# Performance work log

Measured on AMD Instinct MI355X. Metric: run time of the kernel, lower is better.

## Reference

```python
import jax, jax.numpy as jnp
import numpy as np

N_NODES = 100000
N_EDGES = 1600000
N_FEAT = 128
HIDN = 256
N_CLASSES = 47


def setup_inputs() -> dict:
    key = jax.random.key(0)
    ks = jax.random.split(key, 8)
    x = jax.random.normal(ks[0], (N_NODES, N_FEAT), dtype=jnp.float32)
    edge_index = jax.random.randint(ks[1], (2, N_EDGES), 0, N_NODES, dtype=jnp.int32)
    s1 = 1.0 / np.sqrt(N_FEAT)
    s2 = 1.0 / np.sqrt(HIDN)
    Wl1 = jax.random.normal(ks[2], (N_FEAT, HIDN), dtype=jnp.float32) * s1
    Wr1 = jax.random.normal(ks[3], (N_FEAT, HIDN), dtype=jnp.float32) * s1
    b1 = jnp.zeros((HIDN,), dtype=jnp.float32)
    Wl2 = jax.random.normal(ks[4], (HIDN, N_CLASSES), dtype=jnp.float32) * s2
    Wr2 = jax.random.normal(ks[5], (HIDN, N_CLASSES), dtype=jnp.float32) * s2
    b2 = jnp.zeros((N_CLASSES,), dtype=jnp.float32)
    return {"x": x, "edge_index": edge_index, "Wl1": Wl1, "Wr1": Wr1, "b1": b1,
            "Wl2": Wl2, "Wr2": Wr2, "b2": b2}


def _sage_conv(x, src, dst, Wl, Wr, b):
    # PyG SAGEConv (mean aggr): out = lin_l(mean_{j->i} x_j) + lin_r(x_i)
    n = x.shape[0]
    msg = x[src]                                                   # [E, F] gather
    agg = jax.ops.segment_sum(msg, dst, num_segments=n)            # [N, F]
    deg = jax.ops.segment_sum(jnp.ones((src.shape[0], 1), x.dtype), dst,
                              num_segments=n)                      # [N, 1]
    mean = agg / jnp.maximum(deg, 1.0)
    return mean @ Wl + b + x @ Wr


def reference(x, edge_index, Wl1, Wr1, b1, Wl2, Wr2, b2):
    src, dst = edge_index[0], edge_index[1]
    h = _sage_conv(x, src, dst, Wl1, Wr1, b1)
    h = jax.nn.relu(h)
    # dropout omitted (eval mode / deterministic baseline)
    out = _sage_conv(h, src, dst, Wl2, Wr2, b2)
    return out
```

## Files before the change

kernel.cpp:

```cpp
#include <hip/hip_runtime.h>

#define NN 100000
#define NE 1600000
#define NF 128
#define NH 256
#define NC 47
#define NB 391
#define CH 8192
#define NCH ((NE + CH - 1) / CH)

#define PB_HIST 0
#define PB_CAST (PB_HIST + NCH)
#define NCAST   (NN * NF / 4 / 256)
#define PB_BT1  (PB_CAST + NCAST)
#define PB_BT2  (PB_BT1 + 256)
#define PB_END  (PB_BT2 + 96)

typedef __attribute__((ext_vector_type(8))) short bf16x8;
typedef __attribute__((ext_vector_type(4))) float f32x4;
typedef __attribute__((ext_vector_type(2))) float f32x2;

typedef __attribute__((address_space(1))) const void as1_void;
typedef __attribute__((address_space(3))) void as3_void;
__device__ __forceinline__ void gload16(const void* g, void* l) {
    __builtin_amdgcn_global_load_lds((as1_void*)g, (as3_void*)l, 16, 0, 0);
}

__device__ inline unsigned short f2bf(float f) {
    unsigned u = __builtin_bit_cast(unsigned, f);
    unsigned r = u + 0x7fffu + ((u >> 16) & 1u);
    return (unsigned short)(r >> 16);
}
__device__ inline float bfl(unsigned u) {
    return __builtin_bit_cast(float, u << 16);
}


__global__ __launch_bounds__(256) void prep_k(const int* __restrict__ dst,
                                              int* __restrict__ chunk_hist,
                                              int* __restrict__ total,
                                              const float* __restrict__ x,
                                              unsigned short* __restrict__ xb,
                                              unsigned* __restrict__ xq,
                                              const float* __restrict__ Wl1,
                                              const float* __restrict__ Wr1,
                                              unsigned short* __restrict__ Bt1,
                                              const float* __restrict__ Wl2,
                                              const float* __restrict__ Wr2,
                                              unsigned short* __restrict__ Bt2) {
    __shared__ int h[NB];
    int tid = threadIdx.x;
    int blk = blockIdx.x;
    if (blk < PB_CAST) {
        int ch = blk;
        for (int i = tid; i < NB; i += 256) h[i] = 0;
        __syncthreads();
        int e0 = ch * CH;
        int e1 = min(e0 + CH, NE);
        for (int e = e0 + tid; e < e1; e += 256)
            atomicAdd(&h[dst[e] >> 8], 1);
        __syncthreads();
        for (int i = tid; i < NB; i += 256) {
            int v = h[i];
            chunk_hist[(size_t)ch * NB + i] = v;
            if (v) atomicAdd(&total[i], v);
        }
    } else if (blk < PB_BT1) {
        int i = (blk - PB_CAST) * 256 + tid;
        float4 v = *reinterpret_cast<const float4*>(x + (size_t)i * 4);
        ushort4 o;
        o.x = f2bf(v.x); o.y = f2bf(v.y); o.z = f2bf(v.z); o.w = f2bf(v.w);
        *reinterpret_cast<ushort4*>(xb + (size_t)i * 4) = o;
        int r = __builtin_amdgcn_cvt_pk_fp8_f32(v.x, v.y, 0, false);
        r = __builtin_amdgcn_cvt_pk_fp8_f32(v.z, v.w, r, true);
        xq[i] = (unsigned)r;
    } else if (blk < PB_BT2) {
        int idx = (blk - PB_BT1) * 256 + tid;
        int n = idx >> 8, k = idx & 255;
        float v = (k < 128) ? Wl1[(size_t)k * NH + n] : Wr1[(size_t)(k - 128) * NH + n];
        Bt1[idx] = f2bf(v);
    } else {
        int idx = (blk - PB_BT2) * 256 + tid;
        int n = idx >> 8, k = idx & 255;
        float v = 0.f;
        if (n < 47) v = Wl2[(size_t)k * NC + n];
        else if (n >= 48 && n < 95) v = Wr2[(size_t)k * NC + (n - 48)];
        Bt2[idx] = f2bf(v);
    }
}


__global__ __launch_bounds__(64) void scancol_k(const int* __restrict__ chunk_hist,
                                                const int* __restrict__ total,
                                                int* __restrict__ bucket_base,
                                                int* __restrict__ chunk_off) {
    int b = blockIdx.x;
    int lane = threadIdx.x;
    int base = 0;
    for (int i0 = 0; i0 < NB; i0 += 64) {
        int i = i0 + lane;
        base += (i < b) ? total[i] : 0;
    }
    #pragma unroll
    for (int off = 1; off < 64; off <<= 1)
        base += __shfl_xor(base, off);
    if (lane == 0) bucket_base[b] = base;
    int run = base;
    for (int c0 = 0; c0 < NCH; c0 += 64) {
        int c = c0 + lane;
        int v = (c < NCH) ? chunk_hist[(size_t)c * NB + b] : 0;
        int s = v;
        #pragma unroll
        for (int off = 1; off < 64; off <<= 1) {
            int t = __shfl_up(s, off);
            if (lane >= off) s += t;
        }
        if (c < NCH) chunk_off[(size_t)c * NB + b] = run + s - v;
        run += __shfl(s, 63);
    }
}

__global__ __launch_bounds__(256) void scatter2_k(const int* __restrict__ src,
                                                  const int* __restrict__ dst,
                                                  const int* __restrict__ chunk_off,
                                                  unsigned* __restrict__ ebuf) {
    __shared__ int cur[NB];
    int tid = threadIdx.x, ch = blockIdx.x;
    for (int i = tid; i < NB; i += 256)
        cur[i] = chunk_off[(size_t)ch * NB + i];
    __syncthreads();
    int e0 = ch * CH;
    int e1 = min(e0 + CH, NE);
    for (int e = e0 + tid; e < e1; e += 256) {
        int d = dst[e];
        int b = d >> 8;
        int p = atomicAdd(&cur[b], 1);
        ebuf[p] = ((unsigned)(d & 255) << 24) | (unsigned)src[e];
    }
}

__global__ __launch_bounds__(256) void build_csr_k(const unsigned* __restrict__ ebuf,
                                                   const int* __restrict__ bucket_base,
                                                   const int* __restrict__ bucket_cnt,
                                                   int* __restrict__ row_start,
                                                   int* __restrict__ deg,
                                                   float* __restrict__ inv_deg,
                                                   int* __restrict__ csr_src) {
    __shared__ int s[256];
    __shared__ int cursor[256];
    int tid = threadIdx.x;
    int b = blockIdx.x;
    int lo = b << 8;
    int ebase = bucket_base[b];
    int ne = bucket_cnt[b];

    s[tid] = 0;
    __syncthreads();
    for (int e = tid; e < ne; e += 256)
        atomicAdd(&s[ebuf[ebase + e] >> 24], 1);
    __syncthreads();
    int v = s[tid];
    __syncthreads();
    for (int off = 1; off < 256; off <<= 1) {
        int t = (tid >= off) ? s[tid - off] : 0;
        __syncthreads();
        s[tid] += t;
        __syncthreads();
    }
    int excl = s[tid] - v;
    int node = lo + tid;
    if (node < NN) {
        row_start[node] = ebase + excl;
        deg[node] = v;
        inv_deg[node] = 1.0f / (float)(v > 1 ? v : 1);
    }
    cursor[tid] = ebase + excl;
    __syncthreads();
    for (int e = tid; e < ne; e += 256) {
        unsigned u = ebuf[ebase + e];
        int p = atomicAdd(&cursor[u >> 24], 1);
        csr_src[p] = (int)(u & 0xFFFFFFu);
    }
}


__global__ __launch_bounds__(256) void agg_mean_128q_k(const unsigned* __restrict__ xq,
                                                       const int* __restrict__ csr_src,
                                                       const int* __restrict__ row_start,
                                                       const int* __restrict__ deg,
                                                       const float* __restrict__ inv_deg,
                                                       unsigned short* __restrict__ mean1) {
    int node = blockIdx.x * 16 + (threadIdx.x >> 4);
    int l16 = threadIdx.x & 15;
    if (node >= NN) return;
    int s0 = row_start[node];
    int d  = deg[node];
    f32x2 acc[4];
    #pragma unroll
    for (int k = 0; k < 4; ++k) acc[k] = f32x2{0.f, 0.f};
    int j = 0;
    for (; j + 7 < d; j += 8) {
        uint2 w[8];
        #pragma unroll
        for (int r = 0; r < 8; ++r) {
            int s = csr_src[s0 + j + r];
            w[r] = *reinterpret_cast<const uint2*>(xq + (size_t)s * 32 + l16 * 2);
        }
        #pragma unroll
        for (int r = 0; r < 8; ++r) {
            acc[0] += __builtin_amdgcn_cvt_pk_f32_fp8((int)w[r].x, false);
            acc[1] += __builtin_amdgcn_cvt_pk_f32_fp8((int)w[r].x, true);
            acc[2] += __builtin_amdgcn_cvt_pk_f32_fp8((int)w[r].y, false);
            acc[3] += __builtin_amdgcn_cvt_pk_f32_fp8((int)w[r].y, true);
        }
    }
    for (; j + 3 < d; j += 4) {
        uint2 w[4];
        #pragma unroll
        for (int r = 0; r < 4; ++r) {
            int s = csr_src[s0 + j + r];
            w[r] = *reinterpret_cast<const uint2*>(xq + (size_t)s * 32 + l16 * 2);
        }
        #pragma unroll
        for (int r = 0; r < 4; ++r) {
            acc[0] += __builtin_amdgcn_cvt_pk_f32_fp8((int)w[r].x, false);
            acc[1] += __builtin_amdgcn_cvt_pk_f32_fp8((int)w[r].x, true);
            acc[2] += __builtin_amdgcn_cvt_pk_f32_fp8((int)w[r].y, false);
            acc[3] += __builtin_amdgcn_cvt_pk_f32_fp8((int)w[r].y, true);
        }
    }
    for (; j < d; ++j) {
        int s = csr_src[s0 + j];
        uint2 w = *reinterpret_cast<const uint2*>(xq + (size_t)s * 32 + l16 * 2);
        acc[0] += __builtin_amdgcn_cvt_pk_f32_fp8((int)w.x, false);
        acc[1] += __builtin_amdgcn_cvt_pk_f32_fp8((int)w.x, true);
        acc[2] += __builtin_amdgcn_cvt_pk_f32_fp8((int)w.y, false);
        acc[3] += __builtin_amdgcn_cvt_pk_f32_fp8((int)w.y, true);
    }
    float inv = inv_deg[node];
    bf16x8 o;
    #pragma unroll
    for (int k = 0; k < 4; ++k) {
        o[k * 2]     = (short)f2bf(acc[k].x * inv);
        o[k * 2 + 1] = (short)f2bf(acc[k].y * inv);
    }
    *reinterpret_cast<bf16x8*>(mean1 + (size_t)node * NF + l16 * 8) = o;
}

__global__ __launch_bounds__(256) void agg_mean_47q_add_k(const unsigned* __restrict__ tq,
                                                          const int* __restrict__ csr_src,
                                                          const int* __restrict__ row_start,
                                                          const int* __restrict__ deg,
                                                          const float* __restrict__ inv_deg,
                                                          float* __restrict__ out) {
    int node = blockIdx.x * 16 + (threadIdx.x >> 4);
    int l16 = threadIdx.x & 15;
    if (node >= NN) return;
    int s0 = row_start[node];
    int d  = deg[node];
    f32x2 a01 = {0.f, 0.f}, a23 = {0.f, 0.f};
    int j = 0;
    for (; j + 7 < d; j += 8) {
        unsigned w[8];
        #pragma unroll
        for (int r = 0; r < 8; ++r) {
            int s = csr_src[s0 + j + r];
            w[r] = tq[(size_t)s * 16 + l16];
        }
        #pragma unroll
        for (int r = 0; r < 8; ++r) {
            a01 += __builtin_amdgcn_cvt_pk_f32_fp8((int)w[r], false);
            a23 += __builtin_amdgcn_cvt_pk_f32_fp8((int)w[r], true);
        }
    }
    for (; j + 3 < d; j += 4) {
        unsigned w[4];
        #pragma unroll
        for (int r = 0; r < 4; ++r) {
            int s = csr_src[s0 + j + r];
            w[r] = tq[(size_t)s * 16 + l16];
        }
        #pragma unroll
        for (int r = 0; r < 4; ++r) {
            a01 += __builtin_amdgcn_cvt_pk_f32_fp8((int)w[r], false);
            a23 += __builtin_amdgcn_cvt_pk_f32_fp8((int)w[r], true);
        }
    }
    for (; j < d; ++j) {
        int s = csr_src[s0 + j];
        unsigned w = tq[(size_t)s * 16 + l16];
        a01 += __builtin_amdgcn_cvt_pk_f32_fp8((int)w, false);
        a23 += __builtin_amdgcn_cvt_pk_f32_fp8((int)w, true);
    }
    float inv = inv_deg[node];
    int c0 = l16 * 4;
    float vals[4] = {a01.x, a01.y, a23.x, a23.y};
    #pragma unroll
    for (int m = 0; m < 4; ++m) {
        int col = c0 + m;
        if (col < NC) {
            size_t o = (size_t)node * NC + col;
            out[o] += vals[m] * inv;
        }
    }
}


__global__ __launch_bounds__(256, 4) void gemm12_k(const unsigned short* __restrict__ mean1,
                                                   const unsigned short* __restrict__ xb,
                                                   const unsigned short* __restrict__ Bt1,
                                                   const float* __restrict__ b1,
                                                   const unsigned short* __restrict__ Bt2,
                                                   const float* __restrict__ b2,
                                                   unsigned char* __restrict__ tq,
                                                   float* __restrict__ out) {
    __shared__ __align__(16) union SM {
        struct { short As[2][64 * 32]; short Bs[2][256 * 32]; } g;
        unsigned short Hs[64 * 256];
    } sm;
    const int tid = threadIdx.x;
    const int row0 = blockIdx.x * 64;
    const int lane = tid & 63;
    const int wid = tid >> 6;
    const int r15 = lane & 15;
    const int kg = lane >> 4;
    const int swz = (kg ^ ((lane >> 1) & 3)) & 3;

    const int wc = wid;
    f32x4 acc[4][4];
    #pragma unroll
    for (int i = 0; i < 4; ++i)
        #pragma unroll
        for (int j = 0; j < 4; ++j)
            acc[i][j] = f32x4{0.f, 0.f, 0.f, 0.f};

    auto stage = [&](int buf, int kt) {
        {
            int row = tid >> 2, g = tid & 3;
            int grow = row0 + row;
            if (grow >= NN) grow = NN - 1;
            int gs = g ^ ((row >> 1) & 3);
            const unsigned short* asrc = (kt < 128) ? mean1 : xb;
            gload16(asrc + (size_t)grow * NF + (kt & 127) + gs * 8, &sm.g.As[buf][tid * 8]);
        }
        #pragma unroll
        for (int i = 0; i < 4; ++i) {
            int c = tid + i * 256;
            int rn = c >> 2, g = c & 3;
            int gs = g ^ ((rn >> 1) & 3);
            gload16(Bt1 + (size_t)rn * 256 + kt + gs * 8, &sm.g.Bs[buf][c * 8]);
        }
    };
    auto compute = [&](int buf) {
        bf16x8 a[4], b[4];
        #pragma unroll
        for (int mi = 0; mi < 4; ++mi)
            a[mi] = *reinterpret_cast<const bf16x8*>(&sm.g.As[buf][(mi * 16 + r15) * 32 + swz * 8]);
        #pragma unroll
        for (int ni = 0; ni < 4; ++ni)
            b[ni] = *reinterpret_cast<const bf16x8*>(&sm.g.Bs[buf][(wc * 64 + ni * 16 + r15) * 32 + swz * 8]);
        #pragma unroll
        for (int mi = 0; mi < 4; ++mi)
            #pragma unroll
            for (int ni = 0; ni < 4; ++ni)
                acc[mi][ni] = __builtin_amdgcn_mfma_f32_16x16x32_bf16(a[mi], b[ni], acc[mi][ni], 0, 0, 0);
    };

    stage(0, 0);
    __syncthreads();
    int cur = 0;
    #pragma unroll 1
    for (int ks = 0; ks < 8; ++ks) {
        if (ks + 1 < 8) stage(cur ^ 1, (ks + 1) * 32);
        compute(cur);
        __syncthreads();
        cur ^= 1;
    }

    #pragma unroll
    for (int ni = 0; ni < 4; ++ni) {
        int col = wc * 64 + ni * 16 + r15;
        float bias = b1[col];
        int kgrp = col >> 3, within = col & 7;
        #pragma unroll
        for (int mi = 0; mi < 4; ++mi) {
            int rbase = mi * 16 + kg * 4;
            f32x4 c = acc[mi][ni];
            #pragma unroll
            for (int q = 0; q < 4; ++q) {
                int row = rbase + q;
                float v = fmaxf(c[q] + bias, 0.f);
                sm.Hs[row * 256 + (kgrp ^ (row & 31)) * 8 + within] = f2bf(v);
            }
        }
    }
    __syncthreads();

    const int wr2 = wid >> 1, wc2 = wid & 1;
    f32x4 acc2[2][3];
    #pragma unroll
    for (int i = 0; i < 2; ++i)
        #pragma unroll
        for (int j = 0; j < 3; ++j)
            acc2[i][j] = f32x4{0.f, 0.f, 0.f, 0.f};

    #pragma unroll
    for (int kt = 0; kt < 256; kt += 32) {
        bf16x8 a2[2], b2f[3];
        #pragma unroll
        for (int mi = 0; mi < 2; ++mi) {
            int row = wr2 * 32 + mi * 16 + r15;
            int kgrp = (kt >> 3) + kg;
            a2[mi] = *reinterpret_cast<const bf16x8*>(&sm.Hs[row * 256 + (kgrp ^ (row & 31)) * 8]);
        }
        #pragma unroll
        for (int ni = 0; ni < 3; ++ni) {
            int n = wc2 * 48 + ni * 16 + r15;
            b2f[ni] = *reinterpret_cast<const bf16x8*>(Bt2 + (size_t)n * 256 + kt + kg * 8);
        }
        #pragma unroll
        for (int mi = 0; mi < 2; ++mi)
            #pragma unroll
            for (int ni = 0; ni < 3; ++ni)
                acc2[mi][ni] = __builtin_amdgcn_mfma_f32_16x16x32_bf16(a2[mi], b2f[ni], acc2[mi][ni], 0, 0, 0);
    }

    #pragma unroll
    for (int ni = 0; ni < 3; ++ni) {
        int col = wc2 * 48 + ni * 16 + r15;
        float bias = (col >= 48 && col < 95) ? b2[col - 48] : 0.f;
        #pragma unroll
        for (int mi = 0; mi < 2; ++mi) {
            int rbase = row0 + wr2 * 32 + mi * 16 + kg * 4;
            f32x4 c = acc2[mi][ni];
            #pragma unroll
            for (int q = 0; q < 4; ++q) {
                int row = rbase + q;
                if (row < NN) {
                    if (col < 47) {
                        int p = __builtin_amdgcn_cvt_pk_fp8_f32(c[q], c[q], 0, false);
                        tq[(size_t)row * 64 + col] = (unsigned char)(p & 0xFF);
                    } else if (col >= 48 && col < 95) {
                        out[(size_t)row * NC + (col - 48)] = c[q] + bias;
                    }
                }
            }
        }
    }
}


extern "C" void kernel_launch(void* const* d_in, const int* in_sizes, int n_in,
                              void* d_out, int out_size, void* d_ws, size_t ws_size,
                              hipStream_t stream) {
    const float* x    = (const float*)d_in[0];
    const int*   eidx = (const int*)d_in[1];
    const float* Wl1  = (const float*)d_in[2];
    const float* Wr1  = (const float*)d_in[3];
    const float* b1   = (const float*)d_in[4];
    const float* Wl2  = (const float*)d_in[5];
    const float* Wr2  = (const float*)d_in[6];
    const float* b2   = (const float*)d_in[7];
    float* out = (float*)d_out;

    const int* src = eidx;
    const int* dst = eidx + NE;

    size_t off = 0;
    auto alloc = [&](size_t bytes) -> void* {
        void* p = (char*)d_ws + off;
        off += (bytes + 511) & ~(size_t)511;
        return p;
    };
    int*            deg        = (int*)alloc((size_t)NN * 4);
    int*            row_start  = (int*)alloc((size_t)NN * 4);
    float*          inv_deg    = (float*)alloc((size_t)NN * 4);
    int*            csr_src    = (int*)alloc((size_t)NE * 4);
    unsigned*       ebuf       = (unsigned*)alloc((size_t)NE * 4);
    int*            chunk_hist = (int*)alloc((size_t)NCH * NB * 4);
    int*            chunk_off  = (int*)alloc((size_t)NCH * NB * 4);
    int*            bkt_cnt    = (int*)alloc((size_t)NB * 4);
    int*            bkt_base   = (int*)alloc((size_t)NB * 4);
    unsigned short* xb         = (unsigned short*)alloc((size_t)NN * NF * 2);
    unsigned*       xq         = (unsigned*)alloc((size_t)NN * NF);
    unsigned short* mean1      = (unsigned short*)alloc((size_t)NN * NF * 2);
    unsigned char*  tq         = (unsigned char*)alloc((size_t)NN * 64);
    unsigned short* Bt1        = (unsigned short*)alloc((size_t)256 * 256 * 2);
    unsigned short* Bt2        = (unsigned short*)alloc((size_t)96 * 256 * 2);
    (void)ws_size; (void)n_in; (void)in_sizes; (void)out_size;

    hipMemsetAsync(bkt_cnt, 0, (size_t)NB * 4, stream);
    prep_k<<<PB_END, 256, 0, stream>>>(dst, chunk_hist, bkt_cnt,
                                       x, xb, xq, Wl1, Wr1, Bt1, Wl2, Wr2, Bt2);
    scancol_k<<<NB, 64, 0, stream>>>(chunk_hist, bkt_cnt, bkt_base, chunk_off);
    scatter2_k<<<NCH, 256, 0, stream>>>(src, dst, chunk_off, ebuf);
    build_csr_k<<<NB, 256, 0, stream>>>(ebuf, bkt_base, bkt_cnt,
                                        row_start, deg, inv_deg, csr_src);

    agg_mean_128q_k<<<(NN + 15) / 16, 256, 0, stream>>>(xq, csr_src, row_start, deg, inv_deg, mean1);

    gemm12_k<<<(NN + 63) / 64, 256, 0, stream>>>(mean1, xb, Bt1, b1, Bt2, b2, tq, out);

    agg_mean_47q_add_k<<<(NN + 15) / 16, 256, 0, stream>>>((const unsigned*)tq, csr_src, row_start, deg, inv_deg, out);
}
```

Before: 184.5 us.

## Fuse layer-1 mean aggregation into the GEMM kernel via shared memory

```diff
diff --git a/kernel.cpp b/kernel.cpp
--- a/kernel.cpp
+++ b/kernel.cpp
@@ -184,69 +184,6 @@
 }
 
 
-__global__ __launch_bounds__(256) void agg_mean_128q_k(const unsigned* __restrict__ xq,
-                                                       const int* __restrict__ csr_src,
-                                                       const int* __restrict__ row_start,
-                                                       const int* __restrict__ deg,
-                                                       const float* __restrict__ inv_deg,
-                                                       unsigned short* __restrict__ mean1) {
-    int node = blockIdx.x * 16 + (threadIdx.x >> 4);
-    int l16 = threadIdx.x & 15;
-    if (node >= NN) return;
-    int s0 = row_start[node];
-    int d  = deg[node];
-    f32x2 acc[4];
-    #pragma unroll
-    for (int k = 0; k < 4; ++k) acc[k] = f32x2{0.f, 0.f};
-    int j = 0;
-    for (; j + 7 < d; j += 8) {
-        uint2 w[8];
-        #pragma unroll
-        for (int r = 0; r < 8; ++r) {
-            int s = csr_src[s0 + j + r];
-            w[r] = *reinterpret_cast<const uint2*>(xq + (size_t)s * 32 + l16 * 2);
-        }
-        #pragma unroll
-        for (int r = 0; r < 8; ++r) {
-            acc[0] += __builtin_amdgcn_cvt_pk_f32_fp8((int)w[r].x, false);
-            acc[1] += __builtin_amdgcn_cvt_pk_f32_fp8((int)w[r].x, true);
-            acc[2] += __builtin_amdgcn_cvt_pk_f32_fp8((int)w[r].y, false);
-            acc[3] += __builtin_amdgcn_cvt_pk_f32_fp8((int)w[r].y, true);
-        }
-    }
-    for (; j + 3 < d; j += 4) {
-        uint2 w[4];
-        #pragma unroll
-        for (int r = 0; r < 4; ++r) {
-            int s = csr_src[s0 + j + r];
-            w[r] = *reinterpret_cast<const uint2*>(xq + (size_t)s * 32 + l16 * 2);
-        }
-        #pragma unroll
-        for (int r = 0; r < 4; ++r) {
-            acc[0] += __builtin_amdgcn_cvt_pk_f32_fp8((int)w[r].x, false);
-            acc[1] += __builtin_amdgcn_cvt_pk_f32_fp8((int)w[r].x, true);
-            acc[2] += __builtin_amdgcn_cvt_pk_f32_fp8((int)w[r].y, false);
-            acc[3] += __builtin_amdgcn_cvt_pk_f32_fp8((int)w[r].y, true);
-        }
-    }
-    for (; j < d; ++j) {
-        int s = csr_src[s0 + j];
-        uint2 w = *reinterpret_cast<const uint2*>(xq + (size_t)s * 32 + l16 * 2);
-        acc[0] += __builtin_amdgcn_cvt_pk_f32_fp8((int)w.x, false);
-        acc[1] += __builtin_amdgcn_cvt_pk_f32_fp8((int)w.x, true);
-        acc[2] += __builtin_amdgcn_cvt_pk_f32_fp8((int)w.y, false);
-        acc[3] += __builtin_amdgcn_cvt_pk_f32_fp8((int)w.y, true);
-    }
-    float inv = inv_deg[node];
-    bf16x8 o;
-    #pragma unroll
-    for (int k = 0; k < 4; ++k) {
-        o[k * 2]     = (short)f2bf(acc[k].x * inv);
-        o[k * 2 + 1] = (short)f2bf(acc[k].y * inv);
-    }
-    *reinterpret_cast<bf16x8*>(mean1 + (size_t)node * NF + l16 * 8) = o;
-}
-
 __global__ __launch_bounds__(256) void agg_mean_47q_add_k(const unsigned* __restrict__ tq,
                                                           const int* __restrict__ csr_src,
                                                           const int* __restrict__ row_start,
@@ -306,16 +243,20 @@
 }
 
 
-__global__ __launch_bounds__(256, 4) void gemm12_k(const unsigned short* __restrict__ mean1,
-                                                   const unsigned short* __restrict__ xb,
-                                                   const unsigned short* __restrict__ Bt1,
-                                                   const float* __restrict__ b1,
-                                                   const unsigned short* __restrict__ Bt2,
-                                                   const float* __restrict__ b2,
-                                                   unsigned char* __restrict__ tq,
-                                                   float* __restrict__ out) {
+__global__ __launch_bounds__(256, 2) void gemm12f_k(const unsigned* __restrict__ xq,
+                                                    const unsigned short* __restrict__ xb,
+                                                    const int* __restrict__ csr_src,
+                                                    const int* __restrict__ row_start,
+                                                    const int* __restrict__ deg,
+                                                    const float* __restrict__ inv_deg,
+                                                    const unsigned short* __restrict__ Bt1,
+                                                    const float* __restrict__ b1,
+                                                    const unsigned short* __restrict__ Bt2,
+                                                    const float* __restrict__ b2,
+                                                    unsigned char* __restrict__ tq,
+                                                    float* __restrict__ out) {
     __shared__ __align__(16) union SM {
-        struct { short As[2][64 * 32]; short Bs[2][256 * 32]; } g;
+        struct { short Am[4][64 * 32]; short Axb[4][64 * 32]; short Bs[2][256 * 32]; } g;
         unsigned short Hs[64 * 256];
     } sm;
     const int tid = threadIdx.x;
@@ -326,23 +267,92 @@
     const int kg = lane >> 4;
     const int swz = (kg ^ ((lane >> 1) & 3)) & 3;
 
+    {
+        int row = tid >> 2, g = tid & 3;
+        int grow = row0 + row;
+        if (grow >= NN) grow = NN - 1;
+        int gs = g ^ ((row >> 1) & 3);
+        #pragma unroll
+        for (int ts = 0; ts < 4; ++ts)
+            gload16(xb + (size_t)grow * NF + ts * 32 + gs * 8, &sm.g.Axb[ts][tid * 8]);
+    }
+
+    {
+        int grp = tid >> 4, l16 = tid & 15;
+        #pragma unroll 1
+        for (int it = 0; it < 4; ++it) {
+            int nl = grp + it * 16;
+            int node = row0 + nl;
+            f32x2 acc[4];
+            #pragma unroll
+            for (int k = 0; k < 4; ++k) acc[k] = f32x2{0.f, 0.f};
+            float inv = 0.f;
+            if (node < NN) {
+                int s0 = row_start[node];
+                int d  = deg[node];
+                int j = 0;
+                for (; j + 7 < d; j += 8) {
+                    uint2 w[8];
+                    #pragma unroll
+                    for (int r = 0; r < 8; ++r) {
+                        int s = csr_src[s0 + j + r];
+                        w[r] = *reinterpret_cast<const uint2*>(xq + (size_t)s * 32 + l16 * 2);
+                    }
+                    #pragma unroll
+                    for (int r = 0; r < 8; ++r) {
+                        acc[0] += __builtin_amdgcn_cvt_pk_f32_fp8((int)w[r].x, false);
+                        acc[1] += __builtin_amdgcn_cvt_pk_f32_fp8((int)w[r].x, true);
+                        acc[2] += __builtin_amdgcn_cvt_pk_f32_fp8((int)w[r].y, false);
+                        acc[3] += __builtin_amdgcn_cvt_pk_f32_fp8((int)w[r].y, true);
+                    }
+                }
+                for (; j + 3 < d; j += 4) {
+                    uint2 w[4];
+                    #pragma unroll
+                    for (int r = 0; r < 4; ++r) {
+                        int s = csr_src[s0 + j + r];
+                        w[r] = *reinterpret_cast<const uint2*>(xq + (size_t)s * 32 + l16 * 2);
+                    }
+                    #pragma unroll
+                    for (int r = 0; r < 4; ++r) {
+                        acc[0] += __builtin_amdgcn_cvt_pk_f32_fp8((int)w[r].x, false);
+                        acc[1] += __builtin_amdgcn_cvt_pk_f32_fp8((int)w[r].x, true);
+                        acc[2] += __builtin_amdgcn_cvt_pk_f32_fp8((int)w[r].y, false);
+                        acc[3] += __builtin_amdgcn_cvt_pk_f32_fp8((int)w[r].y, true);
+                    }
+                }
+                for (; j < d; ++j) {
+                    int s = csr_src[s0 + j];
+                    uint2 w = *reinterpret_cast<const uint2*>(xq + (size_t)s * 32 + l16 * 2);
+                    acc[0] += __builtin_amdgcn_cvt_pk_f32_fp8((int)w.x, false);
+                    acc[1] += __builtin_amdgcn_cvt_pk_f32_fp8((int)w.x, true);
+                    acc[2] += __builtin_amdgcn_cvt_pk_f32_fp8((int)w.y, false);
+                    acc[3] += __builtin_amdgcn_cvt_pk_f32_fp8((int)w.y, true);
+                }
+                inv = inv_deg[node];
+            }
+            bf16x8 o;
+            #pragma unroll
+            for (int k = 0; k < 4; ++k) {
+                o[k * 2]     = (short)f2bf(acc[k].x * inv);
+                o[k * 2 + 1] = (short)f2bf(acc[k].y * inv);
+            }
+            int ts = l16 >> 2, g = l16 & 3;
+            int slot = g ^ ((nl >> 1) & 3);
+            *reinterpret_cast<bf16x8*>(&sm.g.Am[ts][nl * 32 + slot * 8]) = o;
+        }
+    }
+    __syncthreads();
+
     const int wc = wid;
-    f32x4 acc[4][4];
+    f32x4 acc1[4][4];
     #pragma unroll
     for (int i = 0; i < 4; ++i)
         #pragma unroll
         for (int j = 0; j < 4; ++j)
-            acc[i][j] = f32x4{0.f, 0.f, 0.f, 0.f};
-
-    auto stage = [&](int buf, int kt) {
-        {
-            int row = tid >> 2, g = tid & 3;
-            int grow = row0 + row;
-            if (grow >= NN) grow = NN - 1;
-            int gs = g ^ ((row >> 1) & 3);
-            const unsigned short* asrc = (kt < 128) ? mean1 : xb;
-            gload16(asrc + (size_t)grow * NF + (kt & 127) + gs * 8, &sm.g.As[buf][tid * 8]);
-        }
+            acc1[i][j] = f32x4{0.f, 0.f, 0.f, 0.f};
+
+    auto stageB = [&](int buf, int kt) {
         #pragma unroll
         for (int i = 0; i < 4; ++i) {
             int c = tid + i * 256;
@@ -351,11 +361,12 @@
             gload16(Bt1 + (size_t)rn * 256 + kt + gs * 8, &sm.g.Bs[buf][c * 8]);
         }
     };
-    auto compute = [&](int buf) {
+    auto compute = [&](int buf, int kt) {
+        const short* Abase = (kt < 128) ? sm.g.Am[kt >> 5] : sm.g.Axb[(kt - 128) >> 5];
         bf16x8 a[4], b[4];
         #pragma unroll
         for (int mi = 0; mi < 4; ++mi)
-            a[mi] = *reinterpret_cast<const bf16x8*>(&sm.g.As[buf][(mi * 16 + r15) * 32 + swz * 8]);
+            a[mi] = *reinterpret_cast<const bf16x8*>(&Abase[(mi * 16 + r15) * 32 + swz * 8]);
         #pragma unroll
         for (int ni = 0; ni < 4; ++ni)
             b[ni] = *reinterpret_cast<const bf16x8*>(&sm.g.Bs[buf][(wc * 64 + ni * 16 + r15) * 32 + swz * 8]);
@@ -363,16 +374,16 @@
         for (int mi = 0; mi < 4; ++mi)
             #pragma unroll
             for (int ni = 0; ni < 4; ++ni)
-                acc[mi][ni] = __builtin_amdgcn_mfma_f32_16x16x32_bf16(a[mi], b[ni], acc[mi][ni], 0, 0, 0);
+                acc1[mi][ni] = __builtin_amdgcn_mfma_f32_16x16x32_bf16(a[mi], b[ni], acc1[mi][ni], 0, 0, 0);
     };
 
-    stage(0, 0);
+    stageB(0, 0);
     __syncthreads();
     int cur = 0;
     #pragma unroll 1
     for (int ks = 0; ks < 8; ++ks) {
-        if (ks + 1 < 8) stage(cur ^ 1, (ks + 1) * 32);
-        compute(cur);
+        if (ks + 1 < 8) stageB(cur ^ 1, (ks + 1) * 32);
+        compute(cur, ks * 32);
         __syncthreads();
         cur ^= 1;
     }
@@ -385,7 +396,7 @@
         #pragma unroll
         for (int mi = 0; mi < 4; ++mi) {
             int rbase = mi * 16 + kg * 4;
-            f32x4 c = acc[mi][ni];
+            f32x4 c = acc1[mi][ni];
             #pragma unroll
             for (int q = 0; q < 4; ++q) {
                 int row = rbase + q;
@@ -483,7 +494,6 @@
     int*            bkt_base   = (int*)alloc((size_t)NB * 4);
     unsigned short* xb         = (unsigned short*)alloc((size_t)NN * NF * 2);
     unsigned*       xq         = (unsigned*)alloc((size_t)NN * NF);
-    unsigned short* mean1      = (unsigned short*)alloc((size_t)NN * NF * 2);
     unsigned char*  tq         = (unsigned char*)alloc((size_t)NN * 64);
     unsigned short* Bt1        = (unsigned short*)alloc((size_t)256 * 256 * 2);
     unsigned short* Bt2        = (unsigned short*)alloc((size_t)96 * 256 * 2);
@@ -497,9 +507,8 @@
     build_csr_k<<<NB, 256, 0, stream>>>(ebuf, bkt_base, bkt_cnt,
                                         row_start, deg, inv_deg, csr_src);
 
-    agg_mean_128q_k<<<(NN + 15) / 16, 256, 0, stream>>>(xq, csr_src, row_start, deg, inv_deg, mean1);
-
-    gemm12_k<<<(NN + 63) / 64, 256, 0, stream>>>(mean1, xb, Bt1, b1, Bt2, b2, tq, out);
+    gemm12f_k<<<(NN + 63) / 64, 256, 0, stream>>>(xq, xb, csr_src, row_start, deg, inv_deg,
+                                                  Bt1, b1, Bt2, b2, tq, out);
 
     agg_mean_47q_add_k<<<(NN + 15) / 16, 256, 0, stream>>>((const unsigned*)tq, csr_src, row_start, deg, inv_deg, out);
 }
```

After: 233.0 us. +26.3%, slower.
